# Kernel optimization log

Measured on AMD Instinct MI355X. Metric: run time of the kernel, lower is better.

The kernel has to match this reference:

```python
import jax, jax.numpy as jnp
import numpy as np

D_MODEL = 1024
D_STATE = 16
D_CONV = 4
EXPAND = 2
HEADDIM = 8
D_INNER = EXPAND * D_MODEL            # 2048
NHEADS = D_INNER // HEADDIM           # 256
CONV_DIM = D_INNER + 2 * D_STATE      # 2080 (ngroups=1)
D_IN_PROJ = 2 * D_INNER + 2 * D_STATE + NHEADS  # 4384
B_SZ, SEQ = 4, 2048
EPS = 1e-5


def setup_inputs() -> dict:
    key = jax.random.key(0)
    ks = jax.random.split(key, 8)
    return {
        "x": jax.random.normal(ks[0], (B_SZ, SEQ, D_MODEL), jnp.float32),
        "ln_w": jnp.ones((D_MODEL,), jnp.float32),
        "ln_b": jnp.zeros((D_MODEL,), jnp.float32),
        "W_in": jax.random.normal(ks[1], (D_MODEL, D_IN_PROJ), jnp.float32) * 0.02,
        "conv_w": jax.random.normal(ks[2], (D_CONV, 1, CONV_DIM), jnp.float32) * 0.2,
        "conv_b": jnp.zeros((CONV_DIM,), jnp.float32),
        "A_log": jnp.log(jax.random.uniform(ks[3], (NHEADS,), jnp.float32, 1.0, 16.0)),
        "Dp": jnp.ones((NHEADS,), jnp.float32) + 0.1 * jax.random.normal(ks[4], (NHEADS,), jnp.float32),
        "dt_bias": 0.5 * jax.random.normal(ks[5], (NHEADS,), jnp.float32),
        "rms_w": jnp.ones((D_INNER,), jnp.float32),
        "W_out": jax.random.normal(ks[6], (D_INNER, D_MODEL), jnp.float32) * 0.02,
    }


def _mamba_block(x, ln_w, ln_b, W_in, conv_w, conv_b, A_log, Dp, dt_bias, rms_w, W_out):
    B, L, _ = x.shape
    # pre-norm LayerNorm
    mu = jnp.mean(x, axis=-1, keepdims=True)
    var = jnp.mean((x - mu) ** 2, axis=-1, keepdims=True)
    xn = (x - mu) * jax.lax.rsqrt(var + EPS) * ln_w + ln_b

    # in_proj -> z, xBC, dt
    u = xn @ W_in                                    # (B, L, 4384)
    z = u[..., :D_INNER]
    xBC = u[..., D_INNER:D_INNER + CONV_DIM]
    dt = jax.nn.softplus(u[..., -NHEADS:] + dt_bias)  # (B, L, NHEADS)

    # causal depthwise conv1d + SiLU
    xp = jnp.pad(xBC, ((0, 0), (D_CONV - 1, 0), (0, 0)))
    xBC = jax.lax.conv_general_dilated(
        xp, conv_w, window_strides=(1,), padding="VALID",
        dimension_numbers=("NWC", "WIO", "NWC"), feature_group_count=CONV_DIM)
    xBC = jax.nn.silu(xBC + conv_b)

    xs = xBC[..., :D_INNER].reshape(B, L, NHEADS, HEADDIM)   # SSM input
    Bm = xBC[..., D_INNER:D_INNER + D_STATE]                  # (B, L, N)
    Cm = xBC[..., D_INNER + D_STATE:]                          # (B, L, N)

    A = -jnp.exp(A_log)                                       # (NHEADS,)

    def step(h, inp):
        # h: (B, H, P, N)
        x_t, B_t, C_t, dt_t = inp
        dA = jnp.exp(dt_t * A)                                 # (B, H)
        h = h * dA[..., None, None] + jnp.einsum("bh,bhp,bn->bhpn", dt_t, x_t, B_t)
        y = jnp.einsum("bhpn,bn->bhp", h, C_t)
        return h, y

    h0 = jnp.zeros((B, NHEADS, HEADDIM, D_STATE), x.dtype)
    _, ys = jax.lax.scan(step, h0, (xs.swapaxes(0, 1), Bm.swapaxes(0, 1),
                                     Cm.swapaxes(0, 1), dt.swapaxes(0, 1)))
    y = ys.swapaxes(0, 1) + Dp[None, None, :, None] * xs       # (B, L, H, P)
    y = y.reshape(B, L, D_INNER)

    # gated RMSNorm: rmsnorm(y * silu(z)) * weight
    g = y * jax.nn.silu(z)
    g = g * jax.lax.rsqrt(jnp.mean(g * g, axis=-1, keepdims=True) + EPS) * rms_w

    return x + g @ W_out


def reference(x, ln_w, ln_b, W_in, conv_w, conv_b, A_log, Dp, dt_bias, rms_w, W_out):
    return _mamba_block(x, ln_w, ln_b, W_in, conv_w, conv_b, A_log, Dp, dt_bias, rms_w, W_out)
```

## Files before the change

kernel.cpp:

```cpp
#include <hip/hip_runtime.h>

typedef __bf16 bf16;
typedef __attribute__((ext_vector_type(8))) __bf16 bf16x8;
typedef __attribute__((ext_vector_type(4))) float f32x4;

#define B_SZ 4
#define SEQ 2048
#define DM 1024
#define DIN 2048
#define NH 256
#define DSTATE 16
#define CONVD 2080
#define DPROJ 4384
#define NPAD1 4608
#define MROWS 8192
#define NC 64
#define LC 32
#define UROWB 8768

__device__ __forceinline__ void gload_lds16(const void* g, void* l) {
  __builtin_amdgcn_global_load_lds(
      (__attribute__((address_space(1))) void*)g,
      (__attribute__((address_space(3))) void*)l, 16, 0, 0);
}

template <int N>
__device__ __forceinline__ void vm_wait() {
  asm volatile("s_waitcnt vmcnt(%0)" ::"n"(N) : "memory");
}
__device__ __forceinline__ void bar() { asm volatile("s_barrier" ::: "memory"); }
__device__ __forceinline__ void lgkm0() {
  asm volatile("s_waitcnt lgkmcnt(0)" ::: "memory");
}

__global__ void transpose_cvt(const float* __restrict__ W, bf16* __restrict__ WT,
                              int K, int N, int Npad) {
  __shared__ float tile[32][33];
  int k0 = blockIdx.x * 32, n0 = blockIdx.y * 32;
  int tx = threadIdx.x, ty = threadIdx.y;
#pragma unroll
  for (int j = 0; j < 4; j++) {
    int k = k0 + ty + 8 * j, n = n0 + tx;
    tile[ty + 8 * j][tx] = (k < K && n < N) ? W[(size_t)k * N + n] : 0.f;
  }
  __syncthreads();
#pragma unroll
  for (int j = 0; j < 4; j++) {
    int n = n0 + ty + 8 * j, k = k0 + tx;
    if (n < Npad && k < K) WT[(size_t)n * K + k] = (bf16)tile[tx][ty + 8 * j];
  }
}

__global__ __launch_bounds__(256) void ln_kernel(const float* __restrict__ x,
                                                 const float* __restrict__ lw,
                                                 const float* __restrict__ lb,
                                                 bf16* __restrict__ xn) {
  int row = blockIdx.x;
  int t = threadIdx.x;
  f32x4 v4 = ((const f32x4*)(x + (size_t)row * DM))[t];
  float v0 = v4[0], v1 = v4[1], v2 = v4[2], v3 = v4[3];
  float s = v0 + v1 + v2 + v3;
  float s2 = v0 * v0 + v1 * v1 + v2 * v2 + v3 * v3;
#pragma unroll
  for (int off = 32; off > 0; off >>= 1) {
    s += __shfl_down(s, off);
    s2 += __shfl_down(s2, off);
  }
  __shared__ float ps[8];
  int wave = t >> 6, lane = t & 63;
  if (lane == 0) { ps[wave] = s; ps[4 + wave] = s2; }
  __syncthreads();
  s = ps[0] + ps[1] + ps[2] + ps[3];
  s2 = ps[4] + ps[5] + ps[6] + ps[7];
  float mean = s * (1.f / DM);
  float var = s2 * (1.f / DM) - mean * mean;
  float rstd = rsqrtf(var + 1e-5f);
  f32x4 wv = ((const f32x4*)lw)[t];
  f32x4 bv = ((const f32x4*)lb)[t];
  bf16 o[4];
  o[0] = (bf16)((v0 - mean) * rstd * wv[0] + bv[0]);
  o[1] = (bf16)((v1 - mean) * rstd * wv[1] + bv[1]);
  o[2] = (bf16)((v2 - mean) * rstd * wv[2] + bv[2]);
  o[3] = (bf16)((v3 - mean) * rstd * wv[3] + bv[3]);
  bf16* dst = xn + (size_t)row * DM + t * 4;
  dst[0] = o[0]; dst[1] = o[1]; dst[2] = o[2]; dst[3] = o[3];
}

__global__ __launch_bounds__(512, 2) void gemm1_8p(const bf16* __restrict__ A,
                                                   const bf16* __restrict__ BT,
                                                   bf16* __restrict__ C) {
  __shared__ char lds[131072];
  int bid = blockIdx.x;
  int swz = (bid & 7) * 72 + (bid >> 3);
  int bm = swz / 18, bn = swz - (swz / 18) * 18;
  int m0 = bm * 256, n0 = bn * 256;
  int t = threadIdx.x, lane = t & 63, wave = t >> 6;
  int wm = wave >> 2, wn = wave & 3;
  int lr16 = lane & 15, kq = lane >> 4;
  int ts0 = kq ^ (lr16 & 7);
  int ts1 = (4 + kq) ^ (lr16 & 7);
  int sw = (lane & 7) ^ (lane >> 3);
  int l8 = lane >> 3;
  const char* Ab = (const char*)A;
  const char* Bb = (const char*)BT;

  auto stA = [&](int kt, int p, int h) {
    char* slot = lds + (p * 2 + h) * 16384;
    size_t ko = (size_t)kt * 128 + sw * 16;
#pragma unroll
    for (int g = 0; g < 2; g++) {
      int c = wave * 2 + g;
      int L = c * 8 + l8;
      int grow = m0 + ((L >> 6) << 7) + h * 64 + (L & 63);
      gload_lds16(Ab + (size_t)grow * 2048 + ko, slot + c * 1024);
    }
  };
  auto stB = [&](int kt, int p) {
    char* slot = lds + 65536 + p * 32768;
    size_t ko = (size_t)kt * 128 + sw * 16;
#pragma unroll
    for (int g = 0; g < 4; g++) {
      int c = wave * 4 + g;
      gload_lds16(Bb + (size_t)(n0 + c * 8 + l8) * 2048 + ko, slot + c * 1024);
    }
  };

  f32x4 acc[8][4] = {};
  bf16x8 b_[4][2];
  stA(0, 0, 0); stB(0, 0); stA(0, 0, 1); stA(1, 1, 0); stB(1, 1);
  vm_wait<6>();
  bar();
#pragma unroll 1
  for (int kt = 0; kt < 16; kt++) {
    int p = kt & 1;
    {
      const char* sa_ = lds + (p * 2 + 0) * 16384;
      const char* sb_ = lds + 65536 + p * 32768;
      bf16x8 a_[4][2];
#pragma unroll
      for (int mi = 0; mi < 4; mi++) {
        int lrow = wm * 64 + mi * 16 + lr16;
        a_[mi][0] = *(const bf16x8*)(sa_ + lrow * 128 + ts0 * 16);
        a_[mi][1] = *(const bf16x8*)(sa_ + lrow * 128 + ts1 * 16);
      }
#pragma unroll
      for (int ni = 0; ni < 4; ni++) {
        int lrow = wn * 64 + ni * 16 + lr16;
        b_[ni][0] = *(const bf16x8*)(sb_ + lrow * 128 + ts0 * 16);
        b_[ni][1] = *(const bf16x8*)(sb_ + lrow * 128 + ts1 * 16);
      }
      if (kt < 15) stA(kt + 1, p ^ 1, 1);
      if (kt < 15) vm_wait<8>(); else vm_wait<0>();
      bar();
      lgkm0();
      __builtin_amdgcn_s_setprio(1);
#pragma unroll
      for (int mi = 0; mi < 4; mi++)
#pragma unroll
        for (int ni = 0; ni < 4; ni++) {
          acc[mi][ni] = __builtin_amdgcn_mfma_f32_16x16x32_bf16(a_[mi][0], b_[ni][0], acc[mi][ni], 0, 0, 0);
          acc[mi][ni] = __builtin_amdgcn_mfma_f32_16x16x32_bf16(a_[mi][1], b_[ni][1], acc[mi][ni], 0, 0, 0);
        }
      __builtin_amdgcn_s_setprio(0);
      bar();
    }
    {
      const char* sa_ = lds + (p * 2 + 1) * 16384;
      bf16x8 a_[4][2];
#pragma unroll
      for (int mi = 0; mi < 4; mi++) {
        int lrow = wm * 64 + mi * 16 + lr16;
        a_[mi][0] = *(const bf16x8*)(sa_ + lrow * 128 + ts0 * 16);
        a_[mi][1] = *(const bf16x8*)(sa_ + lrow * 128 + ts1 * 16);
      }
      if (kt < 14) { stA(kt + 2, p, 0); stB(kt + 2, p); }
      if (kt < 14) vm_wait<8>(); else if (kt == 14) vm_wait<2>();
      bar();
      lgkm0();
      __builtin_amdgcn_s_setprio(1);
#pragma unroll
      for (int mi = 0; mi < 4; mi++)
#pragma unroll
        for (int ni = 0; ni < 4; ni++) {
          acc[4 + mi][ni] = __builtin_amdgcn_mfma_f32_16x16x32_bf16(a_[mi][0], b_[ni][0], acc[4 + mi][ni], 0, 0, 0);
          acc[4 + mi][ni] = __builtin_amdgcn_mfma_f32_16x16x32_bf16(a_[mi][1], b_[ni][1], acc[4 + mi][ni], 0, 0, 0);
        }
      __builtin_amdgcn_s_setprio(0);
      bar();
    }
  }
#pragma unroll
  for (int mq = 0; mq < 2; mq++)
#pragma unroll
    for (int mi = 0; mi < 4; mi++)
#pragma unroll
      for (int ni = 0; ni < 4; ni++) {
        int row = m0 + wm * 128 + mq * 64 + mi * 16 + kq * 4;
        int col = n0 + wn * 64 + ni * 16 + lr16;
        f32x4 v = acc[mq * 4 + mi][ni];
        if (col < 4384) {
#pragma unroll
          for (int r = 0; r < 4; r++)
            C[(size_t)(row + r) * DPROJ + col] = (bf16)v[r];
        }
      }
}

#define G2_PHASE(MQ, P, STAGE, VMW)                                                        \
  {                                                                                        \
    const char* sa_ = lds + ((P) * 2 + (MQ)) * 16384;                                      \
    const char* sb_ = lds + 65536 + (P) * 16384;                                           \
    bf16x8 a_[4][2], b_[2][2];                                                             \
    _Pragma("unroll") for (int mi = 0; mi < 4; mi++) {                                     \
      int lrow = wm * 64 + mi * 16 + lr16;                                                 \
      a_[mi][0] = *(const bf16x8*)(sa_ + lrow * 128 + ts0 * 16);                           \
      a_[mi][1] = *(const bf16x8*)(sa_ + lrow * 128 + ts1 * 16);                           \
    }                                                                                      \
    _Pragma("unroll") for (int ni = 0; ni < 2; ni++) {                                     \
      int lrow = wn * 32 + ni * 16 + lr16;                                                 \
      b_[ni][0] = *(const bf16x8*)(sb_ + lrow * 128 + ts0 * 16);                           \
      b_[ni][1] = *(const bf16x8*)(sb_ + lrow * 128 + ts1 * 16);                           \
    }                                                                                      \
    STAGE;                                                                                 \
    VMW;                                                                                   \
    bar();                                                                                 \
    lgkm0();                                                                               \
    __builtin_amdgcn_s_setprio(1);                                                         \
    _Pragma("unroll") for (int mi = 0; mi < 4; mi++)                                       \
      _Pragma("unroll") for (int ni = 0; ni < 2; ni++) {                                   \
        acc[(MQ) * 4 + mi][ni] = __builtin_amdgcn_mfma_f32_16x16x32_bf16(                  \
            a_[mi][0], b_[ni][0], acc[(MQ) * 4 + mi][ni], 0, 0, 0);                        \
        acc[(MQ) * 4 + mi][ni] = __builtin_amdgcn_mfma_f32_16x16x32_bf16(                  \
            a_[mi][1], b_[ni][1], acc[(MQ) * 4 + mi][ni], 0, 0, 0);                        \
      }                                                                                    \
    __builtin_amdgcn_s_setprio(0);                                                         \
    bar();                                                                                 \
  }

__global__ __launch_bounds__(512, 2) void gemm2_8p(const bf16* __restrict__ A,
                                                   const bf16* __restrict__ BT,
                                                   float* __restrict__ C,
                                                   const float* __restrict__ Xres) {
  __shared__ char lds[98304];
  int bid = blockIdx.x;
  int swz = (bid & 7) * 32 + (bid >> 3);
  int bm = swz >> 3, bn = swz & 7;
  int m0 = bm * 256, n0 = bn * 128;
  int t = threadIdx.x, lane = t & 63, wave = t >> 6;
  int wm = wave >> 2, wn = wave & 3;
  int lr16 = lane & 15, kq = lane >> 4;
  int ts0 = kq ^ (lr16 & 7);
  int ts1 = (4 + kq) ^ (lr16 & 7);
  int sw = (lane & 7) ^ ((lane >> 3) & 7);
  int l8 = lane >> 3;
  int c0 = 2 * wave, c1 = 2 * wave + 1;
  int lr0 = c0 * 8 + l8, lr1 = c1 * 8 + l8;
  const char* Ab = (const char*)A;
  const char* Bb = (const char*)BT;
  int grA0 = m0 + (lr0 >> 6) * 128 + (lr0 & 63);
  int grA1 = m0 + (lr1 >> 6) * 128 + (lr1 & 63);
  int gcB0 = n0 + lr0, gcB1 = n0 + lr1;

  auto stA = [&](int kt, int p, int mq) {
    char* slot = lds + (p * 2 + mq) * 16384;
    size_t ko = (size_t)kt * 128 + sw * 16;
    gload_lds16(Ab + (size_t)(grA0 + mq * 64) * 4096 + ko, slot + c0 * 1024);
    gload_lds16(Ab + (size_t)(grA1 + mq * 64) * 4096 + ko, slot + c1 * 1024);
  };
  auto stB = [&](int kt, int p) {
    char* slot = lds + 65536 + p * 16384;
    size_t ko = (size_t)kt * 128 + sw * 16;
    gload_lds16(Bb + (size_t)gcB0 * 4096 + ko, slot + c0 * 1024);
    gload_lds16(Bb + (size_t)gcB1 * 4096 + ko, slot + c1 * 1024);
  };

  f32x4 acc[8][2] = {};
  stA(0, 0, 0); stB(0, 0); stA(0, 0, 1); stA(1, 1, 0);
  vm_wait<4>();
  bar();
#pragma unroll 1
  for (int kt = 0; kt < 32; kt++) {
    int p = kt & 1;
    G2_PHASE(0, p, { if (kt + 1 < 32) { stB(kt + 1, p ^ 1); stA(kt + 1, p ^ 1, 1); } },
             { if (kt < 31) vm_wait<6>(); else vm_wait<0>(); });
    G2_PHASE(1, p, { if (kt + 2 < 32) stA(kt + 2, p, 0); },
             { if (kt < 30) vm_wait<4>(); else if (kt == 30) vm_wait<2>(); });
  }
#pragma unroll
  for (int mq = 0; mq < 2; mq++)
#pragma unroll
    for (int mi = 0; mi < 4; mi++)
#pragma unroll
      for (int ni = 0; ni < 2; ni++) {
        int row = m0 + wm * 128 + mq * 64 + mi * 16 + kq * 4;
        int col = n0 + wn * 32 + ni * 16 + lr16;
        f32x4 v = acc[mq * 4 + mi][ni];
#pragma unroll
        for (int r = 0; r < 4; r++) {
          size_t o = (size_t)(row + r) * DM + col;
          C[o] = Xres[o] + v[r];
        }
      }
}

__global__ __launch_bounds__(256) void conv_prep3(const bf16* __restrict__ u,
                                                  const float* __restrict__ cw,
                                                  const float* __restrict__ cb,
                                                  const float* __restrict__ dt_bias,
                                                  bf16* __restrict__ xs,
                                                  float* __restrict__ BC,
                                                  float* __restrict__ dtf) {
  const int JPR = 292;
  int idx = blockIdx.x * 256 + threadIdx.x;
  if (idx >= MROWS * JPR) return;
  int row = idx / JPR;
  int j = idx - row * JPR;
  int t = row & (SEQ - 1);
  if (j < 260) {
    int c0 = j * 8;
    float acc[8];
#pragma unroll
    for (int i = 0; i < 8; i++) acc[i] = cb[c0 + i];
    const bf16* ub = u + (size_t)row * DPROJ + DIN + c0;
#pragma unroll
    for (int tap = 0; tap < 4; tap++) {
      int tt = t - 3 + tap;
      if (tt >= 0) {
        bf16x8 uv = *(const bf16x8*)(ub + (ptrdiff_t)(tap - 3) * DPROJ);
        const float* wv = cw + tap * CONVD + c0;
#pragma unroll
        for (int i = 0; i < 8; i++) acc[i] += wv[i] * (float)uv[i];
      }
    }
    if (c0 < DIN) {
      bf16x8 o;
#pragma unroll
      for (int i = 0; i < 8; i++) {
        float sv = acc[i] / (1.f + __expf(-acc[i]));
        o[i] = (bf16)sv;
      }
      *(bf16x8*)(xs + (size_t)row * DIN + c0) = o;
    } else {
      float* bc = BC + (size_t)row * 32 + (c0 - DIN);
#pragma unroll
      for (int i = 0; i < 8; i++) bc[i] = acc[i] / (1.f + __expf(-acc[i]));
    }
  } else {
    int h0 = (j - 260) * 8;
    bf16x8 uv = *(const bf16x8*)(u + (size_t)row * DPROJ + (DPROJ - NH) + h0);
    float* dst = dtf + (size_t)row * NH + h0;
#pragma unroll
    for (int i = 0; i < 8; i++) {
      float xv = (float)uv[i] + dt_bias[h0 + i];
      dst[i] = (xv > 20.f) ? xv : log1pf(__expf(xv));
    }
  }
}

__global__ __launch_bounds__(64) void scan_p1(const bf16* __restrict__ xs,
                                              const float* __restrict__ BC,
                                              const float* __restrict__ dtf,
                                              const float* __restrict__ A_log,
                                              bf16* __restrict__ uscr) {
  int c = blockIdx.x & 63, hg = (blockIdx.x >> 6) & 31, b = blockIdx.x >> 11;
  int lane = threadIdx.x, hh = lane >> 3;
  int h = hg * 8 + hh;
  float A = -__expf(A_log[h]);
  float st[16];
#pragma unroll
  for (int n = 0; n < 16; n++) st[n] = 0.f;
  float pcum = 1.f;
  size_t rb = (size_t)b * SEQ + (size_t)c * LC;
  for (int t = 0; t < LC; t++) {
    size_t row = rb + t;
    const float* bcrow = BC + row * 32;
    float dtv = dtf[row * NH + h];
    float x = (float)xs[row * DIN + hg * 64 + lane];
    float dA = __expf(dtv * A);
    pcum *= dA;
    float w = dtv * x;
#pragma unroll
    for (int n = 0; n < 16; n++) st[n] = st[n] * dA + w * bcrow[n];
  }
  char* slot = (char*)uscr + (size_t)blockIdx.x * UROWB + 4096;
  float* S = (float*)slot;
#pragma unroll
  for (int n = 0; n < 16; n++) S[lane * 16 + n] = st[n];
  if ((lane & 7) == 0) ((float*)(slot + 4096))[hh] = pcum;
}

__global__ __launch_bounds__(64) void scan_p2(bf16* __restrict__ uscr) {
  int bh = blockIdx.x;
  int lane = threadIdx.x, hh = lane >> 3;
  float H[16];
#pragma unroll
  for (int n = 0; n < 16; n++) H[n] = 0.f;
  char* base = (char*)uscr + (size_t)bh * NC * UROWB + 4096;
  float sN[16], PN;
  {
    float* S = (float*)base;
#pragma unroll
    for (int n = 0; n < 16; n++) sN[n] = S[lane * 16 + n];
    PN = ((const float*)(base + 4096))[hh];
  }
  for (int c = 0; c < NC; c++) {
    float sC[16], PC = PN;
#pragma unroll
    for (int n = 0; n < 16; n++) sC[n] = sN[n];
    if (c + 1 < NC) {
      char* slot = base + (size_t)(c + 1) * UROWB;
      float* S = (float*)slot;
#pragma unroll
      for (int n = 0; n < 16; n++) sN[n] = S[lane * 16 + n];
      PN = ((const float*)(slot + 4096))[hh];
    }
    float* S0 = (float*)(base + (size_t)c * UROWB);
#pragma unroll
    for (int n = 0; n < 16; n++) {
      float hn = H[n];
      S0[lane * 16 + n] = hn;
      H[n] = PC * hn + sC[n];
    }
  }
}

__global__ __launch_bounds__(64) void scan_p3(const bf16* __restrict__ xs,
                                              const float* __restrict__ BC,
                                              const float* __restrict__ dtf,
                                              const float* __restrict__ A_log,
                                              const float* __restrict__ Dp,
                                              const bf16* __restrict__ uscr,
                                              bf16* __restrict__ y) {
  int c = blockIdx.x & 63, hg = (blockIdx.x >> 6) & 31, b = blockIdx.x >> 11;
  int lane = threadIdx.x, hh = lane >> 3;
  int h = hg * 8 + hh;
  float A = -__expf(A_log[h]);
  float D = Dp[h];
  const char* slot = (const char*)uscr + (size_t)blockIdx.x * UROWB + 4096;
  float st[16];
#pragma unroll
  for (int n = 0; n < 16; n++) st[n] = ((const float*)slot)[lane * 16 + n];
  size_t rb = (size_t)b * SEQ + (size_t)c * LC;
  for (int t = 0; t < LC; t++) {
    size_t row = rb + t;
    const float* bcrow = BC + row * 32;
    float dtv = dtf[row * NH + h];
    float x = (float)xs[row * DIN + hg * 64 + lane];
    float dA = __expf(dtv * A);
    float w = dtv * x;
    float yv = 0.f;
#pragma unroll
    for (int n = 0; n < 16; n++) {
      st[n] = st[n] * dA + w * bcrow[n];
      yv += st[n] * bcrow[16 + n];
    }
    y[row * DIN + hg * 64 + lane] = (bf16)(yv + D * x);
  }
}

__global__ __launch_bounds__(256) void gate_rms(const bf16* __restrict__ u,
                                                const bf16* __restrict__ y,
                                                const float* __restrict__ rms_w,
                                                bf16* __restrict__ g) {
  int row = blockIdx.x;
  int t = threadIdx.x;
  bf16x8 zv = ((const bf16x8*)(u + (size_t)row * DPROJ))[t];
  bf16x8 yv = ((const bf16x8*)(y + (size_t)row * DIN))[t];
  float gv[8];
  float s2 = 0.f;
#pragma unroll
  for (int i = 0; i < 8; i++) {
    float z = (float)zv[i];
    float yy = (float)yv[i];
    float gg = yy * z / (1.f + __expf(-z));
    gv[i] = gg;
    s2 += gg * gg;
  }
#pragma unroll
  for (int off = 32; off > 0; off >>= 1) s2 += __shfl_down(s2, off);
  __shared__ float ps[4];
  int wave = t >> 6, lane = t & 63;
  if (lane == 0) ps[wave] = s2;
  __syncthreads();
  s2 = ps[0] + ps[1] + ps[2] + ps[3];
  float scale = rsqrtf(s2 * (1.f / DIN) + 1e-5f);
  f32x4 w0 = ((const f32x4*)rms_w)[2 * t];
  f32x4 w1 = ((const f32x4*)rms_w)[2 * t + 1];
  bf16x8 og;
#pragma unroll
  for (int i = 0; i < 4; i++) og[i] = (bf16)(gv[i] * scale * w0[i]);
#pragma unroll
  for (int i = 0; i < 4; i++) og[4 + i] = (bf16)(gv[4 + i] * scale * w1[i]);
  ((bf16x8*)(g + (size_t)row * DIN))[t] = og;
}

extern "C" void kernel_launch(void* const* d_in, const int* in_sizes, int n_in,
                              void* d_out, int out_size, void* d_ws, size_t ws_size,
                              hipStream_t stream) {
  const float* x = (const float*)d_in[0];
  const float* lnw = (const float*)d_in[1];
  const float* lnb = (const float*)d_in[2];
  const float* Win = (const float*)d_in[3];
  const float* cw = (const float*)d_in[4];
  const float* cb = (const float*)d_in[5];
  const float* Alog = (const float*)d_in[6];
  const float* Dpv = (const float*)d_in[7];
  const float* dtb = (const float*)d_in[8];
  const float* rmsw = (const float*)d_in[9];
  const float* Wout = (const float*)d_in[10];
  float* out = (float*)d_out;

  char* ws = (char*)d_ws;
  bf16* u = (bf16*)(ws + 0);
  bf16* xnb = (bf16*)(ws + 71827456);
  bf16* WinT = (bf16*)(ws + 88604672);
  bf16* yb = (bf16*)(ws + 71827456);
  bf16* xsb = (bf16*)(ws + 105381888);
  bf16* gb = (bf16*)(ws + 105381888);
  float* BC = (float*)(ws + 138936320);
  float* dtf = (float*)(ws + 139984896);
  bf16* WoutT = (bf16*)(ws + 148373504);

  transpose_cvt<<<dim3(32, 144), dim3(32, 8), 0, stream>>>(Win, WinT, 1024, DPROJ, NPAD1);
  transpose_cvt<<<dim3(64, 32), dim3(32, 8), 0, stream>>>(Wout, WoutT, DIN, DM, DM);
  ln_kernel<<<MROWS, 256, 0, stream>>>(x, lnw, lnb, xnb);
  gemm1_8p<<<576, 512, 0, stream>>>(xnb, WinT, u);
  conv_prep3<<<(MROWS * 292) / 256, 256, 0, stream>>>(u, cw, cb, dtb, xsb, BC, dtf);
  scan_p1<<<MROWS, 64, 0, stream>>>(xsb, BC, dtf, Alog, u);
  scan_p2<<<128, 64, 0, stream>>>(u);
  scan_p3<<<MROWS, 64, 0, stream>>>(xsb, BC, dtf, Alog, Dpv, u, yb);
  gate_rms<<<MROWS, 256, 0, stream>>>(u, yb, rmsw, gb);
  gemm2_8p<<<256, 512, 0, stream>>>(gb, WoutT, out, x);
}
```

Measured before the change: 311.6 us.

## Retile in_proj GEMM to 256x192 with triple-buffered A staging

Changes the in_proj GEMM block tile from 256x256 to 256x192, so the grid becomes 768 blocks, a whole multiple of the CU count, removing the partial last wave. A is now staged as full 256-row tiles in a three-slot ring, and B is double-buffered and loaded one k-step ahead. This reworks the wait counts and barrier placement. LDS use grows to 144KB per block, and each wave now computes a 3-wide N fragment instead of 4, which lowers MFMA work per LDS read of A.

```diff
diff --git a/kernel.cpp b/kernel.cpp
--- a/kernel.cpp
+++ b/kernel.cpp
@@ -89,11 +89,11 @@
 __global__ __launch_bounds__(512, 2) void gemm1_8p(const bf16* __restrict__ A,
                                                    const bf16* __restrict__ BT,
                                                    bf16* __restrict__ C) {
-  __shared__ char lds[131072];
+  __shared__ char lds[147456];
   int bid = blockIdx.x;
-  int swz = (bid & 7) * 72 + (bid >> 3);
-  int bm = swz / 18, bn = swz - (swz / 18) * 18;
-  int m0 = bm * 256, n0 = bn * 256;
+  int swz = (bid & 7) * 96 + (bid >> 3);
+  int bm = swz / 24, bn = swz - (swz / 24) * 24;
+  int m0 = bm * 256, n0 = bn * 192;
   int t = threadIdx.x, lane = t & 63, wave = t >> 6;
   int wm = wave >> 2, wn = wave & 3;
   int lr16 = lane & 15, kq = lane >> 4;
@@ -104,60 +104,59 @@
   const char* Ab = (const char*)A;
   const char* Bb = (const char*)BT;
 
-  auto stA = [&](int kt, int p, int h) {
-    char* slot = lds + (p * 2 + h) * 16384;
+  auto stA = [&](int kt, int ab) {
+    char* slot = lds + ab * 32768;
     size_t ko = (size_t)kt * 128 + sw * 16;
 #pragma unroll
-    for (int g = 0; g < 2; g++) {
-      int c = wave * 2 + g;
-      int L = c * 8 + l8;
-      int grow = m0 + ((L >> 6) << 7) + h * 64 + (L & 63);
-      gload_lds16(Ab + (size_t)grow * 2048 + ko, slot + c * 1024);
+    for (int g = 0; g < 4; g++) {
+      int c = wave * 4 + g;
+      gload_lds16(Ab + (size_t)(m0 + c * 8 + l8) * 2048 + ko, slot + c * 1024);
     }
   };
   auto stB = [&](int kt, int p) {
-    char* slot = lds + 65536 + p * 32768;
+    char* slot = lds + 98304 + p * 24576;
     size_t ko = (size_t)kt * 128 + sw * 16;
 #pragma unroll
-    for (int g = 0; g < 4; g++) {
-      int c = wave * 4 + g;
+    for (int g = 0; g < 3; g++) {
+      int c = wave * 3 + g;
       gload_lds16(Bb + (size_t)(n0 + c * 8 + l8) * 2048 + ko, slot + c * 1024);
     }
   };
 
-  f32x4 acc[8][4] = {};
-  bf16x8 b_[4][2];
-  stA(0, 0, 0); stB(0, 0); stA(0, 0, 1); stA(1, 1, 0); stB(1, 1);
-  vm_wait<6>();
+  f32x4 acc[8][3] = {};
+  bf16x8 a_[4][2], b_[3][2];
+
+  stA(0, 0); stB(0, 0); stA(1, 1);
+  vm_wait<4>();
   bar();
 #pragma unroll 1
   for (int kt = 0; kt < 16; kt++) {
+    int ab = kt % 3;
     int p = kt & 1;
     {
-      const char* sa_ = lds + (p * 2 + 0) * 16384;
-      const char* sb_ = lds + 65536 + p * 32768;
-      bf16x8 a_[4][2];
+      const char* sa = lds + ab * 32768;
+      const char* sb = lds + 98304 + p * 24576;
 #pragma unroll
       for (int mi = 0; mi < 4; mi++) {
-        int lrow = wm * 64 + mi * 16 + lr16;
-        a_[mi][0] = *(const bf16x8*)(sa_ + lrow * 128 + ts0 * 16);
-        a_[mi][1] = *(const bf16x8*)(sa_ + lrow * 128 + ts1 * 16);
-      }
-#pragma unroll
-      for (int ni = 0; ni < 4; ni++) {
-        int lrow = wn * 64 + ni * 16 + lr16;
-        b_[ni][0] = *(const bf16x8*)(sb_ + lrow * 128 + ts0 * 16);
-        b_[ni][1] = *(const bf16x8*)(sb_ + lrow * 128 + ts1 * 16);
-      }
-      if (kt < 15) stA(kt + 1, p ^ 1, 1);
-      if (kt < 15) vm_wait<8>(); else vm_wait<0>();
+        int lrow = wm * 128 + mi * 16 + lr16;
+        a_[mi][0] = *(const bf16x8*)(sa + lrow * 128 + ts0 * 16);
+        a_[mi][1] = *(const bf16x8*)(sa + lrow * 128 + ts1 * 16);
+      }
+#pragma unroll
+      for (int ni = 0; ni < 3; ni++) {
+        int lrow = wn * 48 + ni * 16 + lr16;
+        b_[ni][0] = *(const bf16x8*)(sb + lrow * 128 + ts0 * 16);
+        b_[ni][1] = *(const bf16x8*)(sb + lrow * 128 + ts1 * 16);
+      }
+      if (kt < 15) stB(kt + 1, p ^ 1);
+      if (kt < 14) stA(kt + 2, (kt + 2) % 3);
       bar();
       lgkm0();
       __builtin_amdgcn_s_setprio(1);
 #pragma unroll
       for (int mi = 0; mi < 4; mi++)
 #pragma unroll
-        for (int ni = 0; ni < 4; ni++) {
+        for (int ni = 0; ni < 3; ni++) {
           acc[mi][ni] = __builtin_amdgcn_mfma_f32_16x16x32_bf16(a_[mi][0], b_[ni][0], acc[mi][ni], 0, 0, 0);
           acc[mi][ni] = __builtin_amdgcn_mfma_f32_16x16x32_bf16(a_[mi][1], b_[ni][1], acc[mi][ni], 0, 0, 0);
         }
@@ -165,23 +164,22 @@
       bar();
     }
     {
-      const char* sa_ = lds + (p * 2 + 1) * 16384;
-      bf16x8 a_[4][2];
+      const char* sa = lds + ab * 32768;
 #pragma unroll
       for (int mi = 0; mi < 4; mi++) {
-        int lrow = wm * 64 + mi * 16 + lr16;
-        a_[mi][0] = *(const bf16x8*)(sa_ + lrow * 128 + ts0 * 16);
-        a_[mi][1] = *(const bf16x8*)(sa_ + lrow * 128 + ts1 * 16);
-      }
-      if (kt < 14) { stA(kt + 2, p, 0); stB(kt + 2, p); }
-      if (kt < 14) vm_wait<8>(); else if (kt == 14) vm_wait<2>();
+        int lrow = wm * 128 + 64 + mi * 16 + lr16;
+        a_[mi][0] = *(const bf16x8*)(sa + lrow * 128 + ts0 * 16);
+        a_[mi][1] = *(const bf16x8*)(sa + lrow * 128 + ts1 * 16);
+      }
+      if (kt < 14) vm_wait<4>();
+      else if (kt == 14) vm_wait<0>();
       bar();
       lgkm0();
       __builtin_amdgcn_s_setprio(1);
 #pragma unroll
       for (int mi = 0; mi < 4; mi++)
 #pragma unroll
-        for (int ni = 0; ni < 4; ni++) {
+        for (int ni = 0; ni < 3; ni++) {
           acc[4 + mi][ni] = __builtin_amdgcn_mfma_f32_16x16x32_bf16(a_[mi][0], b_[ni][0], acc[4 + mi][ni], 0, 0, 0);
           acc[4 + mi][ni] = __builtin_amdgcn_mfma_f32_16x16x32_bf16(a_[mi][1], b_[ni][1], acc[4 + mi][ni], 0, 0, 0);
         }
@@ -190,20 +188,18 @@
     }
   }
 #pragma unroll
-  for (int mq = 0; mq < 2; mq++)
-#pragma unroll
-    for (int mi = 0; mi < 4; mi++)
-#pragma unroll
-      for (int ni = 0; ni < 4; ni++) {
-        int row = m0 + wm * 128 + mq * 64 + mi * 16 + kq * 4;
-        int col = n0 + wn * 64 + ni * 16 + lr16;
-        f32x4 v = acc[mq * 4 + mi][ni];
-        if (col < 4384) {
-#pragma unroll
-          for (int r = 0; r < 4; r++)
-            C[(size_t)(row + r) * DPROJ + col] = (bf16)v[r];
-        }
-      }
+  for (int fr = 0; fr < 8; fr++)
+#pragma unroll
+    for (int ni = 0; ni < 3; ni++) {
+      int row = m0 + wm * 128 + fr * 16 + kq * 4;
+      int col = n0 + wn * 48 + ni * 16 + lr16;
+      f32x4 v = acc[fr][ni];
+      if (col < 4384) {
+#pragma unroll
+        for (int r = 0; r < 4; r++)
+          C[(size_t)(row + r) * DPROJ + col] = (bf16)v[r];
+      }
+    }
 }
 
 #define G2_PHASE(MQ, P, STAGE, VMW)                                                        \
@@ -524,7 +520,7 @@
   transpose_cvt<<<dim3(32, 144), dim3(32, 8), 0, stream>>>(Win, WinT, 1024, DPROJ, NPAD1);
   transpose_cvt<<<dim3(64, 32), dim3(32, 8), 0, stream>>>(Wout, WoutT, DIN, DM, DM);
   ln_kernel<<<MROWS, 256, 0, stream>>>(x, lnw, lnb, xnb);
-  gemm1_8p<<<576, 512, 0, stream>>>(xnb, WinT, u);
+  gemm1_8p<<<768, 512, 0, stream>>>(xnb, WinT, u);
   conv_prep3<<<(MROWS * 292) / 256, 256, 0, stream>>>(u, cw, cb, dtb, xsb, BC, dtf);
   scan_p1<<<MROWS, 64, 0, stream>>>(xsb, BC, dtf, Alog, u);
   scan_p2<<<128, 64, 0, stream>>>(u);
```

Measured after the change: 298.6 us. 1.04x faster.
